# Performance work log

Hardware: AMD Instinct MI355X
Metric: run time of the kernel (lower is better)

## Reference

```python
import jax, jax.numpy as jnp
import numpy as np

B, N, M, K = 16, 4096, 512, 16  # batch, input points, fps_num, knn k

def fps(x, m):
    # farthest point sampling: x [B,N,3] -> [B,m,3]
    Bn, Nn, _ = x.shape
    def body(i, state):
        idx, dists, last = state
        d = jnp.sum((x - last[:, None, :]) ** 2, axis=-1)          # [B,N]
        dists = jnp.minimum(dists, d)
        nxt = jnp.argmax(dists, axis=-1).astype(jnp.int32)         # [B]
        idx = idx.at[:, i].set(nxt)
        last = jnp.take_along_axis(x, nxt[:, None, None], axis=1)[:, 0]
        return (idx, dists, last)
    idx0 = jnp.zeros((Bn, m), jnp.int32)
    d0 = jnp.full((Bn, Nn), jnp.inf, x.dtype)
    idx, _, _ = jax.lax.fori_loop(1, m, body, (idx0, d0, x[:, 0]))
    return jnp.take_along_axis(x, idx[:, :, None], axis=1)

def knn_idx(f, k):
    # f: [B,C,N] -> k nearest neighbor indices [B,N,k] (self included)
    sq = jnp.sum(f * f, axis=1)                                     # [B,N]
    d = sq[:, :, None] - 2.0 * jnp.einsum('bcn,bcm->bnm', f, f) + sq[:, None, :]
    return jax.lax.top_k(-d, k)[1]

def gather_nbrs(f, idx):
    # f: [B,C,N], idx: [B,N,k] -> [B,C,N,k]
    return jnp.take_along_axis(f[:, :, :, None], idx[:, None, :, :], axis=2)

def graph_feature(f, k):
    # DGCNN-style edge feature: concat(nbr - center, center) -> [B,2C,N,k]
    idx = knn_idx(f, k)
    fn = gather_nbrs(f, idx)
    fc = jnp.broadcast_to(f[:, :, :, None], fn.shape)
    return jnp.concatenate([fn - fc, fc], axis=1), idx

def c1(W, x):
    # 1x1 conv over [B,C,N,k]
    return jnp.einsum('oc,bcnk->bonk', W, x)

def transformer(x, keyf, pos, idx, Wq, Wk, Wv, P1, P2, A1, A2):
    # point-transformer vector attention over k neighbors
    q = c1(Wq, x); kk = c1(Wk, keyf); v = c1(Wv, keyf)              # [B,D,N,k]
    rel = gather_nbrs(pos, idx) - pos[:, :, :, None]                # [B,3,N,k]
    pe = c1(P2, jax.nn.relu(c1(P1, rel)))                           # [B,D,N,k]
    attn = jax.nn.softmax(c1(A2, jax.nn.relu(c1(A1, q - kk + pe))), axis=-1)
    return jnp.sum(attn * (v + pe), axis=-1)                        # [B,D,N]

def _forward(x, params):
    t1, t2, t3 = params
    partial = jnp.transpose(fps(x, M), (0, 2, 1))                   # [B,3,M]
    gf, idx = graph_feature(partial, K)                             # [B,6,M,K]
    x1 = transformer(gf, gf, partial, idx, *t1)                     # [B,64,M]
    gf, idx = graph_feature(x1, K)                                  # [B,128,M,K]
    x2 = transformer(gf, gf, partial, idx, *t2)                     # [B,64,M]
    gf, idx = graph_feature(x2, K)                                  # [B,128,M,K]
    x3 = transformer(gf, gf, partial, idx, *t3)                     # [B,128,M]
    feat = jnp.concatenate([x1, x2, x3], axis=1)                    # [B,256,M]
    return jnp.concatenate([jnp.max(feat, axis=-1), jnp.mean(feat, axis=-1)], axis=1)  # [B,512]

_SHAPES = {
    't1_Wq': (64, 6), 't1_Wk': (64, 6), 't1_Wv': (64, 6),
    't1_P1': (64, 3), 't1_P2': (64, 64), 't1_A1': (256, 64), 't1_A2': (64, 256),
    't2_Wq': (64, 128), 't2_Wk': (64, 128), 't2_Wv': (64, 128),
    't2_P1': (64, 3), 't2_P2': (64, 64), 't2_A1': (256, 64), 't2_A2': (64, 256),
    't3_Wq': (128, 128), 't3_Wk': (128, 128), 't3_Wv': (128, 128),
    't3_P1': (128, 3), 't3_P2': (128, 128), 't3_A1': (512, 128), 't3_A2': (128, 512),
}

def setup_inputs():
    key = jax.random.key(0)
    inp = {'x': jax.random.normal(key, (B, N, 3), jnp.float32)}
    pkey = jax.random.fold_in(key, 100)
    for i, (name, shp) in enumerate(_SHAPES.items()):
        inp[name] = jax.random.normal(jax.random.fold_in(pkey, i), shp, jnp.float32) * (1.0 / np.sqrt(shp[1]))
    return inp

def reference(x, t1_Wq, t1_Wk, t1_Wv, t1_P1, t1_P2, t1_A1, t1_A2,
              t2_Wq, t2_Wk, t2_Wv, t2_P1, t2_P2, t2_A1, t2_A2,
              t3_Wq, t3_Wk, t3_Wv, t3_P1, t3_P2, t3_A1, t3_A2):
    params = ((t1_Wq, t1_Wk, t1_Wv, t1_P1, t1_P2, t1_A1, t1_A2),
              (t2_Wq, t2_Wk, t2_Wv, t2_P1, t2_P2, t2_A1, t2_A2),
              (t3_Wq, t3_Wk, t3_Wv, t3_P1, t3_P2, t3_A1, t3_A2))
    return _forward(x, params)
```

## Files before the change

### kernel.cpp

```cpp
#include <hip/hip_runtime.h>
#include <cstdint>
#include <cstddef>

#define B_  16
#define N_  4096
#define M_  512
#define KNB 16
#define P_  (B_ * M_)
#define ROWS_ (B_ * M_ * KNB)

typedef unsigned short u16;
typedef unsigned long long u64;
typedef __attribute__((ext_vector_type(4))) unsigned int u32x4;
typedef __attribute__((ext_vector_type(8))) short short8;
typedef __attribute__((ext_vector_type(4))) float f32x4v;

__device__ inline u16 f2bf(float f) {
  union { float f; unsigned u; } x; x.f = f;
  unsigned r = x.u + 0x7fffu + ((x.u >> 16) & 1u);
  return (u16)(r >> 16);
}
__device__ inline float bf2f(u16 h) {
  union { unsigned u; float f; } x; x.u = ((unsigned)h) << 16;
  return x.f;
}

__device__ inline u64 wave_max_u64(u64 k) {
#define STEP64MAX(ctrl)                                                               \
  {                                                                                   \
    unsigned olo = (unsigned)__builtin_amdgcn_update_dpp(0, (int)(unsigned)k, ctrl, 0xf, 0xf, false); \
    unsigned ohi = (unsigned)__builtin_amdgcn_update_dpp(0, (int)(unsigned)(k >> 32), ctrl, 0xf, 0xf, false); \
    u64 o = ((u64)ohi << 32) | olo;                                                   \
    k = o > k ? o : k;                                                                \
  }
  STEP64MAX(0x111) STEP64MAX(0x112) STEP64MAX(0x114) STEP64MAX(0x118)
  STEP64MAX(0x142) STEP64MAX(0x143)
#undef STEP64MAX
  unsigned rlo = (unsigned)__builtin_amdgcn_readlane((int)(unsigned)k, 63);
  unsigned rhi = (unsigned)__builtin_amdgcn_readlane((int)(unsigned)(k >> 32), 63);
  return ((u64)rhi << 32) | rlo;
}
__device__ inline u64 wave_min_u64(u64 k) {
#define STEP64MIN(ctrl)                                                               \
  {                                                                                   \
    unsigned olo = (unsigned)__builtin_amdgcn_update_dpp(-1, (int)(unsigned)k, ctrl, 0xf, 0xf, false); \
    unsigned ohi = (unsigned)__builtin_amdgcn_update_dpp(-1, (int)(unsigned)(k >> 32), ctrl, 0xf, 0xf, false); \
    u64 o = ((u64)ohi << 32) | olo;                                                   \
    k = o < k ? o : k;                                                                \
  }
  STEP64MIN(0x111) STEP64MIN(0x112) STEP64MIN(0x114) STEP64MIN(0x118)
  STEP64MIN(0x142) STEP64MIN(0x143)
#undef STEP64MIN
  unsigned rlo = (unsigned)__builtin_amdgcn_readlane((int)(unsigned)k, 63);
  unsigned rhi = (unsigned)__builtin_amdgcn_readlane((int)(unsigned)(k >> 32), 63);
  return ((u64)rhi << 32) | rlo;
}

__global__ __launch_bounds__(512) void fps_kernel(const float* __restrict__ x,
                                                  float* __restrict__ pts) {
  __shared__ float4 xs4[N_];
  __shared__ __align__(16) u64 rv64[2][8];
  const int b = blockIdx.x, t = threadIdx.x, lane = t & 63, w = t >> 6;
  const float* xb = x + (size_t)b * N_ * 3;
  for (int p = t; p < N_; p += 512) {
    const float* s = xb + p * 3;
    xs4[p] = make_float4(s[0], s[1], s[2], 0.f);
  }
  __syncthreads();

  float px[8], py[8], pz[8], dm[8];
#pragma unroll
  for (int j = 0; j < 8; ++j) {
    float4 v = xs4[t + j * 512];
    px[j] = v.x; py[j] = v.y; pz[j] = v.z;
    dm[j] = __builtin_inff();
  }
  float cx = xs4[0].x, cy = xs4[0].y, cz = xs4[0].z;
  if (t == 0) {
    pts[(size_t)b * M_ * 3 + 0] = cx;
    pts[(size_t)b * M_ * 3 + 1] = cy;
    pts[(size_t)b * M_ * 3 + 2] = cz;
  }
  for (int i = 1; i < M_; ++i) {
    u64 kk8[8];
#pragma unroll
    for (int j = 0; j < 8; ++j) {
      float dx = px[j] - cx, dy = py[j] - cy, dz = pz[j] - cz;
      float dd = __fmul_rn(dx, dx);
      dd = __fadd_rn(dd, __fmul_rn(dy, dy));
      dd = __fadd_rn(dd, __fmul_rn(dz, dz));
      dd = fminf(dm[j], dd);
      dm[j] = dd;
      kk8[j] = ((u64)__float_as_uint(dd) << 32) | (unsigned)(~(t + j * 512));
    }
    u64 k4[4], k2[2], kb;
#pragma unroll
    for (int j = 0; j < 4; ++j) k4[j] = kk8[j] > kk8[j + 4] ? kk8[j] : kk8[j + 4];
#pragma unroll
    for (int j = 0; j < 2; ++j) k2[j] = k4[j] > k4[j + 2] ? k4[j] : k4[j + 2];
    kb = k2[0] > k2[1] ? k2[0] : k2[1];
    kb = wave_max_u64(kb);

    const int par = i & 1;
    if (lane == 0) rv64[par][w] = kb;
    __syncthreads();
    u32x4 a0 = *(const u32x4*)&rv64[par][0];
    u32x4 a1 = *(const u32x4*)&rv64[par][2];
    u32x4 a2 = *(const u32x4*)&rv64[par][4];
    u32x4 a3 = *(const u32x4*)&rv64[par][6];
    u64 q0 = ((u64)a0[1] << 32) | a0[0];
    u64 q1 = ((u64)a0[3] << 32) | a0[2];
    u64 q2 = ((u64)a1[1] << 32) | a1[0];
    u64 q3 = ((u64)a1[3] << 32) | a1[2];
    u64 q4 = ((u64)a2[1] << 32) | a2[0];
    u64 q5 = ((u64)a2[3] << 32) | a2[2];
    u64 q6 = ((u64)a3[1] << 32) | a3[0];
    u64 q7 = ((u64)a3[3] << 32) | a3[2];
    u64 m0 = q0 > q1 ? q0 : q1;
    u64 m1 = q2 > q3 ? q2 : q3;
    u64 m2 = q4 > q5 ? q4 : q5;
    u64 m3 = q6 > q7 ? q6 : q7;
    u64 n0 = m0 > m1 ? m0 : m1;
    u64 n1 = m2 > m3 ? m2 : m3;
    u64 km = n0 > n1 ? n0 : n1;
    int fi = (int)(~(unsigned)km) & (N_ - 1);
    float4 cc = xs4[fi];
    cx = cc.x; cy = cc.y; cz = cc.z;
    if (t == 0) {
      pts[((size_t)b * M_ + i) * 3 + 0] = cx;
      pts[((size_t)b * M_ + i) * 3 + 1] = cy;
      pts[((size_t)b * M_ + i) * 3 + 2] = cz;
    }
  }
}

template <int C>
__global__ __launch_bounds__(256) void knn_kernel(const float* __restrict__ f,
                                                  int* __restrict__ knn) {
  constexpr int C4 = (C + 3) / 4;
  __shared__ float4 ls4[C4 * 513];
  float* lss = (float*)ls4;
  const int b = blockIdx.x >> 4;
  const int mb = (blockIdx.x & 15) * 32;
  const int t = threadIdx.x, lane = t & 63, w = t >> 6;
  const float* fb = f + (size_t)b * M_ * C;
  if (C & 3) {
    for (int j = t; j < M_; j += 256)
      for (int cc = (C & 3); cc < 4; ++cc)
        lss[((C4 - 1) * 513 + j) * 4 + cc] = 0.f;
  }
  for (int s = t; s < M_ * C; s += 256) {
    int j = s / C, c = s % C;
    lss[((c >> 2) * 513 + j) * 4 + (c & 3)] = fb[s];
  }
  __syncthreads();

  float sqj[8];
#pragma unroll
  for (int jj = 0; jj < 8; ++jj) {
    int j = lane + 64 * jj;
    float a = 0.f;
    for (int c4 = 0; c4 < C4; ++c4) {
      float4 v = ls4[c4 * 513 + j];
      a += v.x * v.x + v.y * v.y + v.z * v.z + v.w * v.w;
    }
    sqj[jj] = a;
  }

  for (int rr = 0; rr < 8; ++rr) {
    const int m = mb + w * 8 + rr;
    float sqm = 0.f;
    for (int c4 = 0; c4 < C4; ++c4) {
      float4 v = ls4[c4 * 513 + m];
      sqm += v.x * v.x + v.y * v.y + v.z * v.z + v.w * v.w;
    }
    float dot[8] = {0.f, 0.f, 0.f, 0.f, 0.f, 0.f, 0.f, 0.f};
    for (int c4 = 0; c4 < C4; ++c4) {
      float4 fm = ls4[c4 * 513 + m];
#pragma unroll
      for (int jj = 0; jj < 8; ++jj) {
        float4 fj = ls4[c4 * 513 + lane + 64 * jj];
        dot[jj] += fm.x * fj.x + fm.y * fj.y + fm.z * fj.z + fm.w * fj.w;
      }
    }
    u64 mk[8];
#pragma unroll
    for (int jj = 0; jj < 8; ++jj) {
      float d = (sqm - 2.f * dot[jj]) + sqj[jj];
      unsigned um = __float_as_uint(d);
      um = (um >> 31) ? ~um : (um | 0x80000000u);
      mk[jj] = ((u64)um << 32) | (unsigned)(lane + 64 * jj);
    }

    int* out = knn + ((size_t)b * M_ + m) * KNB;
    for (int kk = 0; kk < KNB; ++kk) {
      u64 k4[4], k2[2], kb;
#pragma unroll
      for (int jj = 0; jj < 4; ++jj) k4[jj] = mk[jj] < mk[jj + 4] ? mk[jj] : mk[jj + 4];
#pragma unroll
      for (int jj = 0; jj < 2; ++jj) k2[jj] = k4[jj] < k4[jj + 2] ? k4[jj] : k4[jj + 2];
      kb = k2[0] < k2[1] ? k2[0] : k2[1];
      kb = wave_min_u64(kb);
#pragma unroll
      for (int jj = 0; jj < 8; ++jj)
        if (mk[jj] == kb) mk[jj] = ~0ull;
      if (lane == 0) out[kk] = (int)(unsigned)kb;
    }
  }
}

__global__ __launch_bounds__(256) void pointproj_kernel(
    const float* __restrict__ f, const float* __restrict__ Wq,
    const float* __restrict__ Wk, const float* __restrict__ Wv,
    float* __restrict__ PC, int C, int D) {
  __shared__ float As[16][68];
  __shared__ float Ws[16][68];
  const int t = threadIdx.x;
  const int r0 = blockIdx.x * 64, n0 = blockIdx.y * 64;
  const int tr = t >> 4, tc = t & 15;
  const int twoC = 2 * C;
  const int fourD = 4 * D;
  float acc[4][4] = {};
  const int Ksteps = (C + 15) / 16;
  for (int ks = 0; ks < Ksteps; ++ks) {
    int k0 = ks * 16;
#pragma unroll
    for (int s = 0; s < 4; ++s) {
      int id = t + s * 256;
      int kk = id & 15, rr = id >> 4;
      int c = k0 + kk;
      As[kk][rr] = (c < C) ? f[(size_t)(r0 + rr) * C + c] : 0.f;
      float wv = 0.f;
      if (c < C) {
        int n = n0 + rr;
        int reg = n / D, d = n % D;
        if (reg == 0)      wv = Wq[d * twoC + c] - Wk[d * twoC + c];
        else if (reg == 1) wv = (Wq[d * twoC + C + c] - Wk[d * twoC + C + c]) -
                                (Wq[d * twoC + c] - Wk[d * twoC + c]);
        else if (reg == 2) wv = Wv[d * twoC + c];
        else               wv = Wv[d * twoC + C + c] - Wv[d * twoC + c];
      }
      Ws[kk][rr] = wv;
    }
    __syncthreads();
#pragma unroll
    for (int kk = 0; kk < 16; ++kk) {
      float4 a = *(const float4*)&As[kk][tr * 4];
      float4 bq = *(const float4*)&Ws[kk][tc * 4];
      acc[0][0] += a.x * bq.x; acc[0][1] += a.x * bq.y; acc[0][2] += a.x * bq.z; acc[0][3] += a.x * bq.w;
      acc[1][0] += a.y * bq.x; acc[1][1] += a.y * bq.y; acc[1][2] += a.y * bq.z; acc[1][3] += a.y * bq.w;
      acc[2][0] += a.z * bq.x; acc[2][1] += a.z * bq.y; acc[2][2] += a.z * bq.z; acc[2][3] += a.z * bq.w;
      acc[3][0] += a.w * bq.x; acc[3][1] += a.w * bq.y; acc[3][2] += a.w * bq.z; acc[3][3] += a.w * bq.w;
    }
    __syncthreads();
  }
  const int col = n0 + tc * 4;
#pragma unroll
  for (int i = 0; i < 4; ++i) {
    int row = r0 + tr * 4 + i;
    float4 o; o.x = acc[i][0]; o.y = acc[i][1]; o.z = acc[i][2]; o.w = acc[i][3];
    *(float4*)&PC[(size_t)row * fourD + col] = o;
  }
}

__global__ void split3_w(const float* __restrict__ Wa, int na, int Ka,
                         const float* __restrict__ Wb, int nb, int Kb,
                         const float* __restrict__ Wc, int nc, int Kc,
                         u16* __restrict__ Ah, u16* __restrict__ Al,
                         u16* __restrict__ Bh, u16* __restrict__ Bl,
                         u16* __restrict__ Ch, u16* __restrict__ Cl) {
  int k = blockIdx.x * 256 + threadIdx.x;
  const float* s; u16 *dh, *dl; int K;
  if (k < na) { s = Wa; dh = Ah; dl = Al; K = Ka; }
  else if ((k -= na) < nb) { s = Wb; dh = Bh; dl = Bl; K = Kb; }
  else if ((k -= nb) < nc) { s = Wc; dh = Ch; dl = Cl; K = Kc; }
  else return;
  int n = k / K, kk = k % K;
  int sw = ((n >> 4) * (K >> 3) + (kk >> 3)) * 128 + (n & 15) * 8 + (kk & 7);
  float v = s[k];
  u16 h = f2bf(v);
  dh[sw] = h;
  dl[sw] = f2bf(v - bf2f(h));
}

template <int D, int H, int RB>
__global__ __launch_bounds__(256) void mega_kernel(
    const float* __restrict__ pts, const float* __restrict__ PC,
    const int* __restrict__ idx, const float* __restrict__ P1,
    const u16* __restrict__ P2h, const u16* __restrict__ P2l,
    const u16* __restrict__ A1h, const u16* __restrict__ A1l,
    const u16* __restrict__ A2h, const u16* __restrict__ A2l,
    float* __restrict__ xout) {
  constexpr int WC = D / 32;
  constexpr int HT = (RB == 64) ? 64 : 128;
  constexpr int WCa = HT / 32;
  constexpr int KCD = D / 8;
  constexpr int KCH = H / 8;
  constexpr int NIT = H / HT;
  constexpr int LSTR = RB + 1;
  constexpr int FD = 4 * D;

  __shared__ u32x4 sh_[KCD * LSTR], sl_[KCD * LSTR];
  __shared__ u32x4 xh_[KCD * LSTR], xl_[KCD * LSTR];
  __shared__ float rel4[RB][4];
  __shared__ int   nps[RB];
  __shared__ float P1s[D][4];

  const int t = threadIdx.x, lane = t & 63, w = t >> 6;
  const int kch = lane >> 4, lrow = lane & 15;
  const int r0g = blockIdx.x * RB;
  const int bm0 = r0g >> 4;

  if (t < RB) {
    int gr = r0g + t;
    int bb = gr >> 13;
    int np = bb * M_ + idx[gr];
    int bm = gr >> 4;
    nps[t] = np;
    rel4[t][0] = pts[np * 3 + 0] - pts[bm * 3 + 0];
    rel4[t][1] = pts[np * 3 + 1] - pts[bm * 3 + 1];
    rel4[t][2] = pts[np * 3 + 2] - pts[bm * 3 + 2];
  }
  for (int e = t; e < D * 4; e += 256) {
    int dd = e >> 2, c = e & 3;
    P1s[dd][c] = (c < 3) ? P1[dd * 3 + c] : 0.f;
  }
  __syncthreads();

  u16* xh_u = (u16*)xh_;
  u16* xl_u = (u16*)xl_;
  u16* sh_u = (u16*)sh_;
  u16* sl_u = (u16*)sl_;

  const int wr2 = (w / WC) * 32, wc2 = (w % WC) * 32;

  float u_r[2][2][4];
#pragma unroll
  for (int fr = 0; fr < 2; ++fr)
#pragma unroll
    for (int fc = 0; fc < 2; ++fc)
#pragma unroll
      for (int q = 0; q < 4; ++q) {
        int row = wr2 + fr * 16 + kch * 4 + q;
        int col = wc2 + fc * 16 + lrow;
        int np = nps[row];
        int bm = bm0 + (row >> 4);
        u_r[fr][fc][q] = PC[(size_t)np * FD + col] + PC[(size_t)bm * FD + D + col];
      }

#pragma unroll
  for (int i = 0; i < RB * D / 256; ++i) {
    int e = t + i * 256;
    int r = e / D, dd = e % D;
    float hh = fmaxf(P1s[dd][0] * rel4[r][0] + P1s[dd][1] * rel4[r][1] +
                     P1s[dd][2] * rel4[r][2], 0.f);
    u16 hi = f2bf(hh), lo = f2bf(hh - bf2f(hi));
    int off = ((dd >> 3) * LSTR + r) * 8 + (dd & 7);
    xh_u[off] = hi; xl_u[off] = lo;
  }
  __syncthreads();

  f32x4v pe_r[2][2];
  {
    f32x4v pac[2][2];
#pragma unroll
    for (int a = 0; a < 2; ++a)
#pragma unroll
      for (int b = 0; b < 2; ++b) pac[a][b] = (f32x4v){0.f, 0.f, 0.f, 0.f};
#pragma unroll
    for (int k0 = 0; k0 < D; k0 += 32) {
      union { u32x4 u; short8 s; } ah[2], al[2], bh[2], bl[2];
#pragma unroll
      for (int fr = 0; fr < 2; ++fr) {
        int ai = ((k0 >> 3) + kch) * LSTR + wr2 + fr * 16 + lrow;
        ah[fr].u = xh_[ai]; al[fr].u = xl_[ai];
      }
#pragma unroll
      for (int fc = 0; fc < 2; ++fc) {
        size_t bi = (size_t)(((wc2 >> 4) + fc) * KCD + (k0 >> 3) + kch) * 128 + lrow * 8;
        bh[fc].u = *(const u32x4*)(P2h + bi);
        bl[fc].u = *(const u32x4*)(P2l + bi);
      }
#pragma unroll
      for (int fr = 0; fr < 2; ++fr)
#pragma unroll
        for (int fc = 0; fc < 2; ++fc) {
          pac[fr][fc] = __builtin_amdgcn_mfma_f32_16x16x32_bf16(ah[fr].s, bh[fc].s, pac[fr][fc], 0, 0, 0);
          pac[fr][fc] = __builtin_amdgcn_mfma_f32_16x16x32_bf16(al[fr].s, bh[fc].s, pac[fr][fc], 0, 0, 0);
          pac[fr][fc] = __builtin_amdgcn_mfma_f32_16x16x32_bf16(ah[fr].s, bl[fc].s, pac[fr][fc], 0, 0, 0);
        }
    }
#pragma unroll
    for (int fr = 0; fr < 2; ++fr)
#pragma unroll
      for (int fc = 0; fc < 2; ++fc) {
        pe_r[fr][fc] = pac[fr][fc];
#pragma unroll
        for (int q = 0; q < 4; ++q) {
          int row = wr2 + fr * 16 + kch * 4 + q;
          int col = wc2 + fc * 16 + lrow;
          float sv = pac[fr][fc][q] + u_r[fr][fc][q];
          u16 hi = f2bf(sv), lo = f2bf(sv - bf2f(hi));
          int off = ((col >> 3) * LSTR + row) * 8 + (col & 7);
          sh_u[off] = hi; sl_u[off] = lo;
        }
      }
  }
  __syncthreads();

  const int wra = (w / WCa) * 32, wca = (w % WCa) * 32;
  f32x4v lac[2][2];
#pragma unroll
  for (int a = 0; a < 2; ++a)
#pragma unroll
    for (int b = 0; b < 2; ++b) lac[a][b] = (f32x4v){0.f, 0.f, 0.f, 0.f};

#pragma unroll 1
  for (int it = 0; it < NIT; ++it) {
    const int hbase = it * HT;
    f32x4v aac[2][2];
#pragma unroll
    for (int a = 0; a < 2; ++a)
#pragma unroll
      for (int b = 0; b < 2; ++b) aac[a][b] = (f32x4v){0.f, 0.f, 0.f, 0.f};
#pragma unroll
    for (int k0 = 0; k0 < D; k0 += 32) {
      union { u32x4 u; short8 s; } ah[2], al[2], bh[2], bl[2];
#pragma unroll
      for (int fr = 0; fr < 2; ++fr) {
        int ai = ((k0 >> 3) + kch) * LSTR + wra + fr * 16 + lrow;
        ah[fr].u = sh_[ai]; al[fr].u = sl_[ai];
      }
#pragma unroll
      for (int fc = 0; fc < 2; ++fc) {
        size_t bi = (size_t)((((hbase + wca) >> 4) + fc) * KCD + (k0 >> 3) + kch) * 128 + lrow * 8;
        bh[fc].u = *(const u32x4*)(A1h + bi);
        bl[fc].u = *(const u32x4*)(A1l + bi);
      }
#pragma unroll
      for (int fr = 0; fr < 2; ++fr)
#pragma unroll
        for (int fc = 0; fc < 2; ++fc) {
          aac[fr][fc] = __builtin_amdgcn_mfma_f32_16x16x32_bf16(ah[fr].s, bh[fc].s, aac[fr][fc], 0, 0, 0);
          aac[fr][fc] = __builtin_amdgcn_mfma_f32_16x16x32_bf16(al[fr].s, bh[fc].s, aac[fr][fc], 0, 0, 0);
          aac[fr][fc] = __builtin_amdgcn_mfma_f32_16x16x32_bf16(ah[fr].s, bl[fc].s, aac[fr][fc], 0, 0, 0);
        }
    }
    __syncthreads();
#pragma unroll
    for (int fr = 0; fr < 2; ++fr)
#pragma unroll
      for (int fc = 0; fc < 2; ++fc)
#pragma unroll
        for (int q = 0; q < 4; ++q) {
          int row = wra + fr * 16 + kch * 4 + q;
          int ch = wca + fc * 16 + lrow;
          float av = fmaxf(aac[fr][fc][q], 0.f);
          u16 hi = f2bf(av), lo = f2bf(av - bf2f(hi));
          int off = ((ch >> 3) * LSTR + row) * 8 + (ch & 7);
          xh_u[off] = hi; xl_u[off] = lo;
        }
    __syncthreads();
#pragma unroll
    for (int k0 = 0; k0 < HT; k0 += 32) {
      union { u32x4 u; short8 s; } ah[2], al[2], bh[2], bl[2];
#pragma unroll
      for (int fr = 0; fr < 2; ++fr) {
        int ai = ((k0 >> 3) + kch) * LSTR + wr2 + fr * 16 + lrow;
        ah[fr].u = xh_[ai]; al[fr].u = xl_[ai];
      }
#pragma unroll
      for (int fc = 0; fc < 2; ++fc) {
        size_t bi = (size_t)(((wc2 >> 4) + fc) * KCH + ((hbase + k0) >> 3) + kch) * 128 + lrow * 8;
        bh[fc].u = *(const u32x4*)(A2h + bi);
        bl[fc].u = *(const u32x4*)(A2l + bi);
      }
#pragma unroll
      for (int fr = 0; fr < 2; ++fr)
#pragma unroll
        for (int fc = 0; fc < 2; ++fc) {
          lac[fr][fc] = __builtin_amdgcn_mfma_f32_16x16x32_bf16(ah[fr].s, bh[fc].s, lac[fr][fc], 0, 0, 0);
          lac[fr][fc] = __builtin_amdgcn_mfma_f32_16x16x32_bf16(al[fr].s, bh[fc].s, lac[fr][fc], 0, 0, 0);
          lac[fr][fc] = __builtin_amdgcn_mfma_f32_16x16x32_bf16(ah[fr].s, bl[fc].s, lac[fr][fc], 0, 0, 0);
        }
    }
  }

#pragma unroll
  for (int fr = 0; fr < 2; ++fr) {
    const int bmg = bm0 + ((wr2 + fr * 16) >> 4);
#pragma unroll
    for (int fc = 0; fc < 2; ++fc) {
      const int col = wc2 + fc * 16 + lrow;
      float lv[4];
#pragma unroll
      for (int q = 0; q < 4; ++q) lv[q] = lac[fr][fc][q];
      float mx = fmaxf(fmaxf(lv[0], lv[1]), fmaxf(lv[2], lv[3]));
      mx = fmaxf(mx, __shfl_xor(mx, 16));
      mx = fmaxf(mx, __shfl_xor(mx, 32));
      float ev[4];
      float ssum = 0.f;
#pragma unroll
      for (int q = 0; q < 4; ++q) { ev[q] = expf(lv[q] - mx); ssum += ev[q]; }
      ssum += __shfl_xor(ssum, 16);
      ssum += __shfl_xor(ssum, 32);
      float acc = 0.f;
#pragma unroll
      for (int q = 0; q < 4; ++q) {
        int row = wr2 + fr * 16 + kch * 4 + q;
        int np = nps[row];
        float vv = PC[(size_t)np * FD + 2 * D + col] + PC[(size_t)bmg * FD + 3 * D + col];
        acc += ev[q] * (vv + pe_r[fr][fc][q]);
      }
      acc += __shfl_xor(acc, 16);
      acc += __shfl_xor(acc, 32);
      if (kch == 0) xout[(size_t)bmg * D + col] = acc / ssum;
    }
  }
}

__global__ __launch_bounds__(256) void final_kernel(const float* __restrict__ x1,
                                                    const float* __restrict__ x2,
                                                    const float* __restrict__ x3,
                                                    float* __restrict__ out) {
  const int b = blockIdx.x, c = threadIdx.x;
  const float* p;
  int D, dc;
  if (c < 64)        { p = x1 + (size_t)b * M_ * 64;  D = 64;  dc = c; }
  else if (c < 128)  { p = x2 + (size_t)b * M_ * 64;  D = 64;  dc = c - 64; }
  else               { p = x3 + (size_t)b * M_ * 128; D = 128; dc = c - 128; }
  float mx = -__builtin_inff(), sm = 0.f;
#pragma unroll 8
  for (int m = 0; m < M_; ++m) {
    float v = p[(size_t)m * D + dc];
    mx = fmaxf(mx, v);
    sm += v;
  }
  out[(size_t)b * 512 + c] = mx;
  out[(size_t)b * 512 + 256 + c] = sm * (1.f / 512.f);
}

extern "C" void kernel_launch(void* const* d_in, const int* in_sizes, int n_in,
                              void* d_out, int out_size, void* d_ws, size_t ws_size,
                              hipStream_t stream) {
  const float* x = (const float*)d_in[0];
  const float* W[21];
  for (int i = 0; i < 21; ++i) W[i] = (const float*)d_in[1 + i];

  float* ws = (float*)d_ws;
  size_t off = 0;
  auto alloc = [&](size_t nfloats) { float* p = ws + off; off += nfloats; return p; };

  float* pts = alloc(24592);
  float* x1  = alloc((size_t)P_ * 64);
  float* x2  = alloc((size_t)P_ * 64);
  float* x3  = alloc((size_t)P_ * 128);
  int*   idxb = (int*)alloc((size_t)P_ * KNB);
  float* PC  = alloc((size_t)P_ * 512);
  u16* P2h = (u16*)alloc(8192);   u16* P2l = (u16*)alloc(8192);
  u16* A1h = (u16*)alloc(32768);  u16* A1l = (u16*)alloc(32768);
  u16* A2h = (u16*)alloc(32768);  u16* A2l = (u16*)alloc(32768);

  fps_kernel<<<B_, 512, 0, stream>>>(x, pts);

  struct Layer {
    const float* f; int C, D, H;
    const float *Wq, *Wk, *Wv, *P1, *P2, *A1, *A2;
    float* xout;
  };
  Layer ls[3] = {
      {pts, 3, 64, 256, W[0], W[1], W[2], W[3], W[4], W[5], W[6], x1},
      {x1, 64, 64, 256, W[7], W[8], W[9], W[10], W[11], W[12], W[13], x2},
      {x2, 64, 128, 512, W[14], W[15], W[16], W[17], W[18], W[19], W[20], x3},
  };

  for (int li = 0; li < 3; ++li) {
    const Layer& L = ls[li];
    if (L.C == 3) knn_kernel<3><<<B_ * 16, 256, 0, stream>>>(L.f, idxb);
    else          knn_kernel<64><<<B_ * 16, 256, 0, stream>>>(L.f, idxb);

    pointproj_kernel<<<dim3(P_ / 64, 4 * L.D / 64), 256, 0, stream>>>(
        L.f, L.Wq, L.Wk, L.Wv, PC, L.C, L.D);

    int nP2 = L.D * L.D, nA1 = L.H * L.D, nA2 = L.D * L.H;
    split3_w<<<(nP2 + nA1 + nA2 + 255) / 256, 256, 0, stream>>>(
        L.P2, nP2, L.D, L.A1, nA1, L.D, L.A2, nA2, L.H,
        P2h, P2l, A1h, A1l, A2h, A2l);

    if (L.D == 64)
      mega_kernel<64, 256, 64><<<ROWS_ / 64, 256, 0, stream>>>(
          pts, PC, idxb, L.P1, P2h, P2l, A1h, A1l, A2h, A2l, L.xout);
    else
      mega_kernel<128, 512, 32><<<ROWS_ / 32, 256, 0, stream>>>(
          pts, PC, idxb, L.P1, P2h, P2l, A1h, A1l, A2h, A2l, L.xout);
  }

  final_kernel<<<B_, 256, 0, stream>>>(x1, x2, x3, (float*)d_out);
}
```

Before: 1.008 ms.

## Use 1024-thread FPS blocks with shared-memory atomicMax triple-buffered reduction

The farthest-point-sampling kernel now runs 1024 threads per batch block, with 4 points per thread instead of 8. The cross-wave argmax no longer writes per-wave slots that every thread reads back and reduces. Instead each wave's lane 0 does a 64-bit atomicMax into one of three rotating LDS cells, so only one barrier is needed per iteration. This shortens the per-thread serial chain in a latency-bound loop of 511 iterations, at the cost of 16 serialized LDS atomics and a wider block barrier.

```diff
diff --git a/kernel.cpp b/kernel.cpp
--- a/kernel.cpp
+++ b/kernel.cpp
@@ -56,22 +56,23 @@
   return ((u64)rhi << 32) | rlo;
 }
 
-__global__ __launch_bounds__(512) void fps_kernel(const float* __restrict__ x,
-                                                  float* __restrict__ pts) {
+__global__ __launch_bounds__(1024) void fps_kernel(const float* __restrict__ x,
+                                                   float* __restrict__ pts) {
   __shared__ float4 xs4[N_];
-  __shared__ __align__(16) u64 rv64[2][8];
-  const int b = blockIdx.x, t = threadIdx.x, lane = t & 63, w = t >> 6;
+  __shared__ u64 cell[3];
+  const int b = blockIdx.x, t = threadIdx.x, lane = t & 63;
   const float* xb = x + (size_t)b * N_ * 3;
-  for (int p = t; p < N_; p += 512) {
+  for (int p = t; p < N_; p += 1024) {
     const float* s = xb + p * 3;
     xs4[p] = make_float4(s[0], s[1], s[2], 0.f);
   }
+  if (t < 3) cell[t] = 0;
   __syncthreads();
 
-  float px[8], py[8], pz[8], dm[8];
-#pragma unroll
-  for (int j = 0; j < 8; ++j) {
-    float4 v = xs4[t + j * 512];
+  float px[4], py[4], pz[4], dm[4];
+#pragma unroll
+  for (int j = 0; j < 4; ++j) {
+    float4 v = xs4[t + j * 1024];
     px[j] = v.x; py[j] = v.y; pz[j] = v.z;
     dm[j] = __builtin_inff();
   }
@@ -82,47 +83,28 @@
     pts[(size_t)b * M_ * 3 + 2] = cz;
   }
   for (int i = 1; i < M_; ++i) {
-    u64 kk8[8];
-#pragma unroll
-    for (int j = 0; j < 8; ++j) {
+    u64 kk[4];
+#pragma unroll
+    for (int j = 0; j < 4; ++j) {
       float dx = px[j] - cx, dy = py[j] - cy, dz = pz[j] - cz;
       float dd = __fmul_rn(dx, dx);
       dd = __fadd_rn(dd, __fmul_rn(dy, dy));
       dd = __fadd_rn(dd, __fmul_rn(dz, dz));
       dd = fminf(dm[j], dd);
       dm[j] = dd;
-      kk8[j] = ((u64)__float_as_uint(dd) << 32) | (unsigned)(~(t + j * 512));
-    }
-    u64 k4[4], k2[2], kb;
-#pragma unroll
-    for (int j = 0; j < 4; ++j) k4[j] = kk8[j] > kk8[j + 4] ? kk8[j] : kk8[j + 4];
-#pragma unroll
-    for (int j = 0; j < 2; ++j) k2[j] = k4[j] > k4[j + 2] ? k4[j] : k4[j + 2];
-    kb = k2[0] > k2[1] ? k2[0] : k2[1];
+      kk[j] = ((u64)__float_as_uint(dd) << 32) | (unsigned)(~(t + j * 1024));
+    }
+    u64 ka = kk[0] > kk[2] ? kk[0] : kk[2];
+    u64 kc = kk[1] > kk[3] ? kk[1] : kk[3];
+    u64 kb = ka > kc ? ka : kc;
     kb = wave_max_u64(kb);
 
-    const int par = i & 1;
-    if (lane == 0) rv64[par][w] = kb;
+    const int par = i % 3;
+    if (lane == 0)
+      atomicMax((unsigned long long*)&cell[par], (unsigned long long)kb);
     __syncthreads();
-    u32x4 a0 = *(const u32x4*)&rv64[par][0];
-    u32x4 a1 = *(const u32x4*)&rv64[par][2];
-    u32x4 a2 = *(const u32x4*)&rv64[par][4];
-    u32x4 a3 = *(const u32x4*)&rv64[par][6];
-    u64 q0 = ((u64)a0[1] << 32) | a0[0];
-    u64 q1 = ((u64)a0[3] << 32) | a0[2];
-    u64 q2 = ((u64)a1[1] << 32) | a1[0];
-    u64 q3 = ((u64)a1[3] << 32) | a1[2];
-    u64 q4 = ((u64)a2[1] << 32) | a2[0];
-    u64 q5 = ((u64)a2[3] << 32) | a2[2];
-    u64 q6 = ((u64)a3[1] << 32) | a3[0];
-    u64 q7 = ((u64)a3[3] << 32) | a3[2];
-    u64 m0 = q0 > q1 ? q0 : q1;
-    u64 m1 = q2 > q3 ? q2 : q3;
-    u64 m2 = q4 > q5 ? q4 : q5;
-    u64 m3 = q6 > q7 ? q6 : q7;
-    u64 n0 = m0 > m1 ? m0 : m1;
-    u64 n1 = m2 > m3 ? m2 : m3;
-    u64 km = n0 > n1 ? n0 : n1;
+    u64 km = cell[par];
+    if (t == 0) cell[(par + 2) % 3] = 0;
     int fi = (int)(~(unsigned)km) & (N_ - 1);
     float4 cc = xs4[fi];
     cx = cc.x; cy = cc.y; cz = cc.z;
@@ -561,7 +543,7 @@
   u16* A1h = (u16*)alloc(32768);  u16* A1l = (u16*)alloc(32768);
   u16* A2h = (u16*)alloc(32768);  u16* A2l = (u16*)alloc(32768);
 
-  fps_kernel<<<B_, 512, 0, stream>>>(x, pts);
+  fps_kernel<<<B_, 1024, 0, stream>>>(x, pts);
 
   struct Layer {
     const float* f; int C, D, H;
```

Result: slower. 1.043 ms (+3.5%).
